# Performance work log

Hardware: AMD Instinct MI355X
Metric: run time of the kernel (lower is better)

The kernel has to match this reference:

```python
import jax, jax.numpy as jnp
import numpy as np

N_NODES = 100000
N_EDGES = 1600000
N_GRAPHS = 1000
X_S = 128
HID = 64


def setup_inputs() -> dict:
    key = jax.random.key(0)
    ks = jax.random.split(key, 12)
    x = jax.random.normal(ks[0], (N_NODES, X_S), dtype=jnp.float32)
    edge_index = jax.random.randint(ks[1], (2, N_EDGES), 0, N_NODES, dtype=jnp.int64)
    batch = jnp.sort(jax.random.randint(ks[2], (N_NODES,), 0, N_GRAPHS, dtype=jnp.int64))
    def lin(k, fin, fout):
        s = 1.0 / np.sqrt(fin)
        kw, kb = jax.random.split(k)
        W = jax.random.uniform(kw, (fin, fout), minval=-s, maxval=s, dtype=jnp.float32)
        b = jax.random.uniform(kb, (fout,), minval=-s, maxval=s, dtype=jnp.float32)
        return W, b
    W1, b1 = lin(ks[3], X_S, HID)
    W2, b2 = lin(ks[4], HID, HID)
    W3, b3 = lin(ks[5], HID, HID)
    Wf, bf = lin(ks[6], HID, 10)
    Wl, bl = lin(ks[7], 10, 1)
    eps1 = jnp.float32(0.37)
    eps2 = jnp.float32(0.72)
    eps3 = jnp.float32(0.11)
    return {"x": x, "edge_index": edge_index, "batch": batch,
            "W1": W1, "b1": b1, "W2": W2, "b2": b2, "W3": W3, "b3": b3,
            "Wf": Wf, "bf": bf, "Wl": Wl, "bl": bl,
            "eps1": eps1, "eps2": eps2, "eps3": eps3}


def _gin_conv(h, src, dst, eps, W, b):
    # GIN: nn((1+eps)*x_i + sum_{j in N(i)} x_j); messages flow src -> dst
    agg = jax.ops.segment_sum(h[src], dst, num_segments=N_NODES)  # [N, d]
    return ((1.0 + eps) * h + agg) @ W + b


def reference(x, edge_index, batch, W1, b1, W2, b2, W3, b3, Wf, bf, Wl, bl,
              eps1, eps2, eps3):
    src, dst = edge_index[0], edge_index[1]
    h = jax.nn.relu(_gin_conv(x, src, dst, eps1, W1, b1))
    h = jax.nn.relu(_gin_conv(h, src, dst, eps2, W2, b2))
    h = jax.nn.relu(_gin_conv(h, src, dst, eps3, W3, b3))
    # global_mean_pool over graph ids
    sums = jax.ops.segment_sum(h, batch, num_segments=N_GRAPHS)        # [G, 64]
    cnts = jax.ops.segment_sum(jnp.ones((N_NODES,), h.dtype), batch,
                               num_segments=N_GRAPHS)                   # [G]
    pooled = sums / jnp.maximum(cnts, 1.0)[:, None]
    out = jax.nn.relu(pooled @ Wf + bf) @ Wl + bl                       # [G, 1]
    return out
```

## Files before the change

### kernel.cpp

```cpp
#include <hip/hip_runtime.h>

#define N_NODES 100000
#define N_EDGES 1600000
#define N_GRAPHS 1000

#define NB_C 782
#define B1   256
#define CHUNK (N_EDGES / B1)
#define MTOT (NB_C * B1)

#define LSTR 68

typedef unsigned int uint32;
typedef unsigned short ushort16;

static __device__ __forceinline__ ushort16 f2bf(float f) {
    uint32 u = __float_as_uint(f);
    u += 0x7fffu + ((u >> 16) & 1u);
    return (ushort16)(u >> 16);
}
static __device__ __forceinline__ uint32 pk2(float a, float b) {
    return (uint32)f2bf(a) | ((uint32)f2bf(b) << 16);
}
static __device__ __forceinline__ void bf2x(uint32 v, float& lo, float& hi) {
    lo = __uint_as_float(v << 16);
    hi = __uint_as_float(v & 0xffff0000u);
}


__global__ __launch_bounds__(256) void count_kernel(
    const int* __restrict__ dst, int* __restrict__ M)
{
    __shared__ int cnt[NB_C];
    int b = blockIdx.x, t = threadIdx.x;
    for (int q = t; q < NB_C; q += 256) cnt[q] = 0;
    __syncthreads();
    int e0 = b * CHUNK;
    for (int e = e0 + t; e < e0 + CHUNK; e += 256)
        atomicAdd(&cnt[dst[e] >> 7], 1);
    __syncthreads();
    for (int q = t; q < NB_C; q += 256) M[q * B1 + b] = cnt[q];
}

#define SCAN_B 1024
#define SCAN_NBLK ((MTOT + SCAN_B - 1) / SCAN_B)

__global__ __launch_bounds__(256) void scanA_kernel(
    const int* __restrict__ in, int* __restrict__ excl, int* __restrict__ bsum)
{
    __shared__ int s[256];
    int b = blockIdx.x, t = threadIdx.x;
    int base = b * SCAN_B + t * 4;
    int v[4];
#pragma unroll
    for (int i = 0; i < 4; ++i) v[i] = (base + i < MTOT) ? in[base + i] : 0;
    int tsum = v[0] + v[1] + v[2] + v[3];
    s[t] = tsum;
    __syncthreads();
    for (int off = 1; off < 256; off <<= 1) {
        int x = (t >= off) ? s[t - off] : 0;
        __syncthreads();
        s[t] += x;
        __syncthreads();
    }
    int run = s[t] - tsum;
#pragma unroll
    for (int i = 0; i < 4; ++i) {
        if (base + i < MTOT) excl[base + i] = run;
        run += v[i];
    }
    if (t == 255) bsum[b] = s[255];
}

__global__ __launch_bounds__(256) void scanB_kernel(int* __restrict__ bsum)
{
    __shared__ int s[256];
    int t = threadIdx.x;
    int v = (t < SCAN_NBLK) ? bsum[t] : 0;
    s[t] = v;
    __syncthreads();
    for (int off = 1; off < 256; off <<= 1) {
        int x = (t >= off) ? s[t - off] : 0;
        __syncthreads();
        s[t] += x;
        __syncthreads();
    }
    if (t < SCAN_NBLK) bsum[t] = s[t] - v;
}

__global__ __launch_bounds__(256) void scanC_kernel(
    const int* __restrict__ excl, const int* __restrict__ bsum,
    int* __restrict__ out)
{
    int b = blockIdx.x, t = threadIdx.x;
    int add = bsum[b];
    int base = b * SCAN_B + t * 4;
#pragma unroll
    for (int i = 0; i < 4; ++i)
        if (base + i < MTOT) out[base + i] = excl[base + i] + add;
}

__global__ __launch_bounds__(256) void scatter_kernel(
    const int* __restrict__ src, const int* __restrict__ dst,
    const int* __restrict__ Ms, uint32* __restrict__ tmp)
{
    __shared__ int cur[NB_C];
    int b = blockIdx.x, t = threadIdx.x;
    for (int q = t; q < NB_C; q += 256) cur[q] = Ms[q * B1 + b];
    __syncthreads();
    int e0 = b * CHUNK;
    for (int e = e0 + t; e < e0 + CHUNK; e += 256) {
        int d = dst[e];
        int q = d >> 7;
        int pos = atomicAdd(&cur[q], 1);
        tmp[pos] = ((uint32)(d & 127) << 17) | (uint32)src[e];
    }
}

__global__ __launch_bounds__(256) void finalize_kernel(
    const uint32* __restrict__ tmp, const int* __restrict__ Ms,
    int* __restrict__ row_off, int* __restrict__ esrc)
{
    __shared__ int cnt[128];
    __shared__ int pref[128];
    __shared__ int cur[128];
    int q = blockIdx.x, t = threadIdx.x;
    int start = Ms[q * B1];
    int end = (q == NB_C - 1) ? N_EDGES : Ms[(q + 1) * B1];

    if (t < 128) cnt[t] = 0;
    __syncthreads();
    for (int e = start + t; e < end; e += 256)
        atomicAdd(&cnt[tmp[e] >> 17], 1);
    __syncthreads();
    if (t < 128) pref[t] = cnt[t];
    __syncthreads();
    for (int off = 1; off < 128; off <<= 1) {
        int x = 0;
        if (t < 128 && t >= off) x = pref[t - off];
        __syncthreads();
        if (t < 128) pref[t] += x;
        __syncthreads();
    }
    if (t < 128) {
        int excl = pref[t] - cnt[t];
        int node = q * 128 + t;
        if (node < N_NODES) row_off[node] = start + excl;
        cur[t] = start + excl;
    }
    if (q == 0 && t == 0) row_off[N_NODES] = N_EDGES;
    __syncthreads();
    for (int e = start + t; e < end; e += 256) {
        uint32 u = tmp[e];
        int pos = atomicAdd(&cur[u >> 17], 1);
        esrc[pos] = (int)(u & 0x1FFFFu);
    }
}

template<int IN>
__global__ __launch_bounds__(256) void gemm_kernel(
    const float* __restrict__ h,
    const float* __restrict__ W,
    ushort16* __restrict__ y)
{
    __shared__ float hs[64 * LSTR];

    const int t = threadIdx.x;
    const int node0 = blockIdx.x * 64;
    const int m = t >> 4;
    const int p = t & 15;

    float4 acc[4];
#pragma unroll
    for (int i = 0; i < 4; ++i) acc[i] = make_float4(0.f, 0.f, 0.f, 0.f);

    for (int kb = 0; kb < IN / 64; ++kb) {
        if (kb) __syncthreads();
        {
            int kc = (t & 15) * 4;
            int rbase = t >> 4;
#pragma unroll
            for (int rr = 0; rr < 4; ++rr) {
                int row = rr * 16 + rbase;
                int node = node0 + row;
                float4 v = make_float4(0.f, 0.f, 0.f, 0.f);
                if (node < N_NODES)
                    v = *(const float4*)&h[(size_t)node * IN + kb * 64 + kc];
                *(float4*)&hs[row * LSTR + kc] = v;
            }
        }
        __syncthreads();

        const float* hb = &hs[(m * 4) * LSTR];
        const float* Wb = W + (size_t)(kb * 64) * 64 + p * 4;
#pragma unroll 4
        for (int kc = 0; kc < 64; kc += 4) {
            float4 hv[4];
#pragma unroll
            for (int i = 0; i < 4; ++i) hv[i] = *(const float4*)&hb[i * LSTR + kc];
            float4 w0 = *(const float4*)&Wb[(kc + 0) * 64];
            float4 w1 = *(const float4*)&Wb[(kc + 1) * 64];
            float4 w2 = *(const float4*)&Wb[(kc + 2) * 64];
            float4 w3 = *(const float4*)&Wb[(kc + 3) * 64];
#pragma unroll
            for (int i = 0; i < 4; ++i) {
                acc[i].x = fmaf(hv[i].x, w0.x, acc[i].x);
                acc[i].y = fmaf(hv[i].x, w0.y, acc[i].y);
                acc[i].z = fmaf(hv[i].x, w0.z, acc[i].z);
                acc[i].w = fmaf(hv[i].x, w0.w, acc[i].w);
                acc[i].x = fmaf(hv[i].y, w1.x, acc[i].x);
                acc[i].y = fmaf(hv[i].y, w1.y, acc[i].y);
                acc[i].z = fmaf(hv[i].y, w1.z, acc[i].z);
                acc[i].w = fmaf(hv[i].y, w1.w, acc[i].w);
                acc[i].x = fmaf(hv[i].z, w2.x, acc[i].x);
                acc[i].y = fmaf(hv[i].z, w2.y, acc[i].y);
                acc[i].z = fmaf(hv[i].z, w2.z, acc[i].z);
                acc[i].w = fmaf(hv[i].z, w2.w, acc[i].w);
                acc[i].x = fmaf(hv[i].w, w3.x, acc[i].x);
                acc[i].y = fmaf(hv[i].w, w3.y, acc[i].y);
                acc[i].z = fmaf(hv[i].w, w3.z, acc[i].z);
                acc[i].w = fmaf(hv[i].w, w3.w, acc[i].w);
            }
        }
    }

#pragma unroll
    for (int i = 0; i < 4; ++i) {
        int node = node0 + m * 4 + i;
        if (node >= N_NODES) continue;
        *(uint2*)&y[(size_t)node * 64 + p * 4] =
            make_uint2(pk2(acc[i].x, acc[i].y), pk2(acc[i].z, acc[i].w));
    }
}

__global__ __launch_bounds__(256) void gemm_bf16_kernel(
    const uint32* __restrict__ hb,
    const float* __restrict__ W,
    ushort16* __restrict__ y)
{
    __shared__ float hs[64 * LSTR];

    const int t = threadIdx.x;
    const int node0 = blockIdx.x * 64;

    {
        int w = t & 7;
        int rbase = t >> 3;
#pragma unroll
        for (int rr = 0; rr < 2; ++rr) {
            int row = rr * 32 + rbase;
            int node = node0 + row;
            uint4 v = make_uint4(0u, 0u, 0u, 0u);
            if (node < N_NODES)
                v = *(const uint4*)&hb[(size_t)node * 32 + w * 4];
            float f[8];
            bf2x(v.x, f[0], f[1]);
            bf2x(v.y, f[2], f[3]);
            bf2x(v.z, f[4], f[5]);
            bf2x(v.w, f[6], f[7]);
            float* o = &hs[row * LSTR + w * 8];
            *(float4*)o       = make_float4(f[0], f[1], f[2], f[3]);
            *(float4*)(o + 4) = make_float4(f[4], f[5], f[6], f[7]);
        }
    }
    __syncthreads();

    const int m = t >> 4;
    const int p = t & 15;
    float4 acc[4];
#pragma unroll
    for (int i = 0; i < 4; ++i) acc[i] = make_float4(0.f, 0.f, 0.f, 0.f);

    const float* hbp = &hs[(m * 4) * LSTR];
    const float* Wb = W + p * 4;
#pragma unroll 4
    for (int kc = 0; kc < 64; kc += 4) {
        float4 hv[4];
#pragma unroll
        for (int i = 0; i < 4; ++i) hv[i] = *(const float4*)&hbp[i * LSTR + kc];
        float4 w0 = *(const float4*)&Wb[(kc + 0) * 64];
        float4 w1 = *(const float4*)&Wb[(kc + 1) * 64];
        float4 w2 = *(const float4*)&Wb[(kc + 2) * 64];
        float4 w3 = *(const float4*)&Wb[(kc + 3) * 64];
#pragma unroll
        for (int i = 0; i < 4; ++i) {
            acc[i].x = fmaf(hv[i].x, w0.x, acc[i].x);
            acc[i].y = fmaf(hv[i].x, w0.y, acc[i].y);
            acc[i].z = fmaf(hv[i].x, w0.z, acc[i].z);
            acc[i].w = fmaf(hv[i].x, w0.w, acc[i].w);
            acc[i].x = fmaf(hv[i].y, w1.x, acc[i].x);
            acc[i].y = fmaf(hv[i].y, w1.y, acc[i].y);
            acc[i].z = fmaf(hv[i].y, w1.z, acc[i].z);
            acc[i].w = fmaf(hv[i].y, w1.w, acc[i].w);
            acc[i].x = fmaf(hv[i].z, w2.x, acc[i].x);
            acc[i].y = fmaf(hv[i].z, w2.y, acc[i].y);
            acc[i].z = fmaf(hv[i].z, w2.z, acc[i].z);
            acc[i].w = fmaf(hv[i].z, w2.w, acc[i].w);
            acc[i].x = fmaf(hv[i].w, w3.x, acc[i].x);
            acc[i].y = fmaf(hv[i].w, w3.y, acc[i].y);
            acc[i].z = fmaf(hv[i].w, w3.z, acc[i].z);
            acc[i].w = fmaf(hv[i].w, w3.w, acc[i].w);
        }
    }

#pragma unroll
    for (int i = 0; i < 4; ++i) {
        int node = node0 + m * 4 + i;
        if (node >= N_NODES) continue;
        *(uint2*)&y[(size_t)node * 64 + p * 4] =
            make_uint2(pk2(acc[i].x, acc[i].y), pk2(acc[i].z, acc[i].w));
    }
}

__global__ __launch_bounds__(256) void aggregate_kernel(
    const uint32* __restrict__ y,
    const int* __restrict__ row_off,
    const int* __restrict__ esrc,
    const float* __restrict__ b,
    const float* __restrict__ eps_p,
    uint32* __restrict__ outb)
{
    int lane = threadIdx.x & 63;
    int wave = threadIdx.x >> 6;
    int g = lane >> 4;
    int j = (lane >> 3) & 1;
    int w = lane & 7;
    int node = blockIdx.x * 16 + wave * 4 + g;

    int s0 = row_off[node], s1 = row_off[node + 1];
    float a[8], c[8];
#pragma unroll
    for (int i = 0; i < 8; ++i) { a[i] = 0.f; c[i] = 0.f; }

    const uint32* yw = y + (size_t)w * 4;
    int e = s0 + j;
    for (; e + 2 < s1; e += 4) {
        int i0 = esrc[e];
        int i1 = esrc[e + 2];
        uint4 v0 = *(const uint4*)&yw[(size_t)i0 * 32];
        uint4 v1 = *(const uint4*)&yw[(size_t)i1 * 32];
        float lo, hi;
        bf2x(v0.x, lo, hi); a[0] += lo; a[1] += hi;
        bf2x(v0.y, lo, hi); a[2] += lo; a[3] += hi;
        bf2x(v0.z, lo, hi); a[4] += lo; a[5] += hi;
        bf2x(v0.w, lo, hi); a[6] += lo; a[7] += hi;
        bf2x(v1.x, lo, hi); c[0] += lo; c[1] += hi;
        bf2x(v1.y, lo, hi); c[2] += lo; c[3] += hi;
        bf2x(v1.z, lo, hi); c[4] += lo; c[5] += hi;
        bf2x(v1.w, lo, hi); c[6] += lo; c[7] += hi;
    }
    if (e < s1) {
        int i0 = esrc[e];
        uint4 v0 = *(const uint4*)&yw[(size_t)i0 * 32];
        float lo, hi;
        bf2x(v0.x, lo, hi); a[0] += lo; a[1] += hi;
        bf2x(v0.y, lo, hi); a[2] += lo; a[3] += hi;
        bf2x(v0.z, lo, hi); a[4] += lo; a[5] += hi;
        bf2x(v0.w, lo, hi); a[6] += lo; a[7] += hi;
    }
#pragma unroll
    for (int i = 0; i < 8; ++i) {
        a[i] += c[i];
        a[i] += __shfl_xor(a[i], 8);
    }

    if (j == 0) {
        uint4 sv = *(const uint4*)&yw[(size_t)node * 32];
        float s[8];
        bf2x(sv.x, s[0], s[1]);
        bf2x(sv.y, s[2], s[3]);
        bf2x(sv.z, s[4], s[5]);
        bf2x(sv.w, s[6], s[7]);
        float ep1 = 1.0f + eps_p[0];
        float4 b0 = *(const float4*)&b[w * 8];
        float4 b1 = *(const float4*)&b[w * 8 + 4];
        float r0 = fmaxf(fmaf(ep1, s[0], a[0]) + b0.x, 0.0f);
        float r1 = fmaxf(fmaf(ep1, s[1], a[1]) + b0.y, 0.0f);
        float r2 = fmaxf(fmaf(ep1, s[2], a[2]) + b0.z, 0.0f);
        float r3 = fmaxf(fmaf(ep1, s[3], a[3]) + b0.w, 0.0f);
        float r4 = fmaxf(fmaf(ep1, s[4], a[4]) + b1.x, 0.0f);
        float r5 = fmaxf(fmaf(ep1, s[5], a[5]) + b1.y, 0.0f);
        float r6 = fmaxf(fmaf(ep1, s[6], a[6]) + b1.z, 0.0f);
        float r7 = fmaxf(fmaf(ep1, s[7], a[7]) + b1.w, 0.0f);
        *(uint4*)&outb[(size_t)node * 32 + w * 4] =
            make_uint4(pk2(r0, r1), pk2(r2, r3), pk2(r4, r5), pk2(r6, r7));
    }
}

__global__ __launch_bounds__(256) void pool_head_kernel(
    const uint32* __restrict__ hb,
    const int* __restrict__ batch,
    const float* __restrict__ Wf,
    const float* __restrict__ bfv,
    const float* __restrict__ Wl,
    const float* __restrict__ blv,
    float* __restrict__ out)
{
    __shared__ float red[4][64];
    __shared__ float pooled[64];
    __shared__ float hid[10];
    int g = blockIdx.x;
    int t = threadIdx.x;
    int lo = 0, hi = N_NODES;
    while (lo < hi) { int mid = (lo + hi) >> 1; if (batch[mid] < g) lo = mid + 1; else hi = mid; }
    int start = lo;
    hi = N_NODES;
    while (lo < hi) { int mid = (lo + hi) >> 1; if (batch[mid] < g + 1) lo = mid + 1; else hi = mid; }
    int end = lo;

    int c = t & 63, nl = t >> 6;
    int wd = c >> 1, odd = c & 1;
    float acc = 0.0f;
    for (int i = start + nl; i < end; i += 4) {
        uint32 u = hb[(size_t)i * 32 + wd];
        acc += __uint_as_float(odd ? (u & 0xffff0000u) : (u << 16));
    }
    red[nl][c] = acc;
    __syncthreads();
    if (t < 64) {
        float cnt = (float)(end - start);
        float inv = 1.0f / fmaxf(cnt, 1.0f);
        pooled[t] = (red[0][t] + red[1][t] + red[2][t] + red[3][t]) * inv;
    }
    __syncthreads();
    if (t < 10) {
        float s = bfv[t];
#pragma unroll
        for (int k = 0; k < 64; ++k) s = fmaf(pooled[k], Wf[k * 10 + t], s);
        hid[t] = fmaxf(s, 0.0f);
    }
    __syncthreads();
    if (t == 0) {
        float s = blv[0];
#pragma unroll
        for (int j = 0; j < 10; ++j) s = fmaf(hid[j], Wl[j], s);
        out[g] = s;
    }
}

extern "C" void kernel_launch(void* const* d_in, const int* in_sizes, int n_in,
                              void* d_out, int out_size, void* d_ws, size_t ws_size,
                              hipStream_t stream)
{
    const float* x     = (const float*)d_in[0];
    const int*   ei    = (const int*)  d_in[1];
    const int*   src   = ei;
    const int*   dst   = ei + N_EDGES;
    const int*   batch = (const int*)  d_in[2];
    const float* W1    = (const float*)d_in[3];
    const float* b1    = (const float*)d_in[4];
    const float* W2    = (const float*)d_in[5];
    const float* b2    = (const float*)d_in[6];
    const float* W3    = (const float*)d_in[7];
    const float* b3    = (const float*)d_in[8];
    const float* Wf    = (const float*)d_in[9];
    const float* bfv   = (const float*)d_in[10];
    const float* Wl    = (const float*)d_in[11];
    const float* blv   = (const float*)d_in[12];
    const float* eps1  = (const float*)d_in[13];
    const float* eps2  = (const float*)d_in[14];
    const float* eps3  = (const float*)d_in[15];

    ushort16* ybA = (ushort16*)d_ws;
    ushort16* ybB = ybA + (size_t)N_NODES * 64;
    int*   ints = (int*)(ybB + (size_t)N_NODES * 64);
    int*   M       = ints;
    int*   Mex     = M + MTOT;
    int*   Ms      = Mex + MTOT;
    int*   bsum    = Ms + MTOT;
    int*   row_off = bsum + 256;
    int*   esrc    = row_off + N_NODES + 1;
    uint32* tmp    = (uint32*)(esrc + N_EDGES);

    count_kernel<<<B1, 256, 0, stream>>>(dst, M);
    scanA_kernel<<<SCAN_NBLK, 256, 0, stream>>>(M, Mex, bsum);
    scanB_kernel<<<1, 256, 0, stream>>>(bsum);
    scanC_kernel<<<SCAN_NBLK, 256, 0, stream>>>(Mex, bsum, Ms);
    scatter_kernel<<<B1, 256, 0, stream>>>(src, dst, Ms, tmp);
    finalize_kernel<<<NB_C, 256, 0, stream>>>(tmp, Ms, row_off, esrc);

    const int gemm_blk = (N_NODES + 63) / 64;
    const int agg_blk  = N_NODES / 16;

    gemm_kernel<128><<<gemm_blk, 256, 0, stream>>>(x, W1, ybA);
    aggregate_kernel<<<agg_blk, 256, 0, stream>>>(
        (const uint32*)ybA, row_off, esrc, b1, eps1, (uint32*)ybB);

    gemm_bf16_kernel<<<gemm_blk, 256, 0, stream>>>((const uint32*)ybB, W2, ybA);
    aggregate_kernel<<<agg_blk, 256, 0, stream>>>(
        (const uint32*)ybA, row_off, esrc, b2, eps2, (uint32*)ybB);

    gemm_bf16_kernel<<<gemm_blk, 256, 0, stream>>>((const uint32*)ybB, W3, ybA);
    aggregate_kernel<<<agg_blk, 256, 0, stream>>>(
        (const uint32*)ybA, row_off, esrc, b3, eps3, (uint32*)ybB);

    pool_head_kernel<<<N_GRAPHS, 256, 0, stream>>>(
        (const uint32*)ybB, batch, Wf, bfv, Wl, blv, (float*)d_out);
}
```

Measured before the change: 352.7 us.

## Use bf16 MFMA instructions for the three GIN layer GEMMs

Replaces the FP32 FMA-based shared-memory GEMM kernels with wave-level 16x16x32 bf16 MFMA kernels that load operands directly into registers. A small preliminary kernel converts and transposes W1..W3 into bf16 workspace buffers so B fragments can be loaded contiguously. The first layer now rounds x to bf16 before multiplying, which adds precision loss, and output stores become scattered 2-byte writes instead of packed vector stores.

```diff
diff --git a/kernel.cpp b/kernel.cpp
--- a/kernel.cpp
+++ b/kernel.cpp
@@ -9,10 +9,10 @@
 #define CHUNK (N_EDGES / B1)
 #define MTOT (NB_C * B1)
 
-#define LSTR 68
-
 typedef unsigned int uint32;
 typedef unsigned short ushort16;
+typedef __attribute__((ext_vector_type(8))) short short8;
+typedef __attribute__((ext_vector_type(4))) float f32x4;
 
 static __device__ __forceinline__ ushort16 f2bf(float f) {
     uint32 u = __float_as_uint(f);
@@ -25,6 +25,33 @@
 static __device__ __forceinline__ void bf2x(uint32 v, float& lo, float& hi) {
     lo = __uint_as_float(v << 16);
     hi = __uint_as_float(v & 0xffff0000u);
+}
+
+union CV8 { uint4 u; short8 s; };
+
+__global__ __launch_bounds__(256) void convw_kernel(
+    const float* __restrict__ W1, const float* __restrict__ W2,
+    const float* __restrict__ W3,
+    ushort16* __restrict__ W1t, ushort16* __restrict__ W2t,
+    ushort16* __restrict__ W3t)
+{
+    int t = threadIdx.x;
+    if (blockIdx.x == 0) {
+        for (int i = t; i < 64 * 128; i += 256) {
+            int j = i >> 7, k = i & 127;
+            W1t[i] = f2bf(W1[k * 64 + j]);
+        }
+    } else if (blockIdx.x == 1) {
+        for (int i = t; i < 64 * 64; i += 256) {
+            int j = i >> 6, k = i & 63;
+            W2t[i] = f2bf(W2[k * 64 + j]);
+        }
+    } else {
+        for (int i = t; i < 64 * 64; i += 256) {
+            int j = i >> 6, k = i & 63;
+            W3t[i] = f2bf(W3[k * 64 + j]);
+        }
+    }
 }
 
 
@@ -157,159 +184,104 @@
     }
 }
 
-template<int IN>
-__global__ __launch_bounds__(256) void gemm_kernel(
-    const float* __restrict__ h,
-    const float* __restrict__ W,
+__global__ __launch_bounds__(256) void gemm1_mfma_kernel(
+    const float* __restrict__ x,
+    const ushort16* __restrict__ Wt,
     ushort16* __restrict__ y)
 {
-    __shared__ float hs[64 * LSTR];
-
-    const int t = threadIdx.x;
-    const int node0 = blockIdx.x * 64;
-    const int m = t >> 4;
-    const int p = t & 15;
-
-    float4 acc[4];
-#pragma unroll
-    for (int i = 0; i < 4; ++i) acc[i] = make_float4(0.f, 0.f, 0.f, 0.f);
-
-    for (int kb = 0; kb < IN / 64; ++kb) {
-        if (kb) __syncthreads();
-        {
-            int kc = (t & 15) * 4;
-            int rbase = t >> 4;
-#pragma unroll
-            for (int rr = 0; rr < 4; ++rr) {
-                int row = rr * 16 + rbase;
-                int node = node0 + row;
-                float4 v = make_float4(0.f, 0.f, 0.f, 0.f);
-                if (node < N_NODES)
-                    v = *(const float4*)&h[(size_t)node * IN + kb * 64 + kc];
-                *(float4*)&hs[row * LSTR + kc] = v;
-            }
-        }
-        __syncthreads();
-
-        const float* hb = &hs[(m * 4) * LSTR];
-        const float* Wb = W + (size_t)(kb * 64) * 64 + p * 4;
-#pragma unroll 4
-        for (int kc = 0; kc < 64; kc += 4) {
-            float4 hv[4];
-#pragma unroll
-            for (int i = 0; i < 4; ++i) hv[i] = *(const float4*)&hb[i * LSTR + kc];
-            float4 w0 = *(const float4*)&Wb[(kc + 0) * 64];
-            float4 w1 = *(const float4*)&Wb[(kc + 1) * 64];
-            float4 w2 = *(const float4*)&Wb[(kc + 2) * 64];
-            float4 w3 = *(const float4*)&Wb[(kc + 3) * 64];
-#pragma unroll
-            for (int i = 0; i < 4; ++i) {
-                acc[i].x = fmaf(hv[i].x, w0.x, acc[i].x);
-                acc[i].y = fmaf(hv[i].x, w0.y, acc[i].y);
-                acc[i].z = fmaf(hv[i].x, w0.z, acc[i].z);
-                acc[i].w = fmaf(hv[i].x, w0.w, acc[i].w);
-                acc[i].x = fmaf(hv[i].y, w1.x, acc[i].x);
-                acc[i].y = fmaf(hv[i].y, w1.y, acc[i].y);
-                acc[i].z = fmaf(hv[i].y, w1.z, acc[i].z);
-                acc[i].w = fmaf(hv[i].y, w1.w, acc[i].w);
-                acc[i].x = fmaf(hv[i].z, w2.x, acc[i].x);
-                acc[i].y = fmaf(hv[i].z, w2.y, acc[i].y);
-                acc[i].z = fmaf(hv[i].z, w2.z, acc[i].z);
-                acc[i].w = fmaf(hv[i].z, w2.w, acc[i].w);
-                acc[i].x = fmaf(hv[i].w, w3.x, acc[i].x);
-                acc[i].y = fmaf(hv[i].w, w3.y, acc[i].y);
-                acc[i].z = fmaf(hv[i].w, w3.z, acc[i].z);
-                acc[i].w = fmaf(hv[i].w, w3.w, acc[i].w);
-            }
-        }
-    }
-
-#pragma unroll
-    for (int i = 0; i < 4; ++i) {
-        int node = node0 + m * 4 + i;
-        if (node >= N_NODES) continue;
-        *(uint2*)&y[(size_t)node * 64 + p * 4] =
-            make_uint2(pk2(acc[i].x, acc[i].y), pk2(acc[i].z, acc[i].w));
-    }
-}
-
-__global__ __launch_bounds__(256) void gemm_bf16_kernel(
-    const uint32* __restrict__ hb,
-    const float* __restrict__ W,
+    int lane = threadIdx.x & 63;
+    int wave = threadIdx.x >> 6;
+    int col = lane & 15, quad = lane >> 4;
+    int node0 = blockIdx.x * 64 + wave * 16;
+    int anode = node0 + col;
+
+    short8 a[4];
+    if (anode < N_NODES) {
+        const float* xr = &x[(size_t)anode * 128 + quad * 8];
+#pragma unroll
+        for (int s = 0; s < 4; ++s) {
+            float4 v0 = *(const float4*)&xr[s * 32];
+            float4 v1 = *(const float4*)&xr[s * 32 + 4];
+            CV8 cv;
+            cv.u = make_uint4(pk2(v0.x, v0.y), pk2(v0.z, v0.w),
+                              pk2(v1.x, v1.y), pk2(v1.z, v1.w));
+            a[s] = cv.s;
+        }
+    } else {
+        short8 z = {0, 0, 0, 0, 0, 0, 0, 0};
+#pragma unroll
+        for (int s = 0; s < 4; ++s) a[s] = z;
+    }
+
+    f32x4 acc[4];
+#pragma unroll
+    for (int nt = 0; nt < 4; ++nt)
+#pragma unroll
+        for (int r = 0; r < 4; ++r) acc[nt][r] = 0.0f;
+
+#pragma unroll
+    for (int nt = 0; nt < 4; ++nt) {
+        const ushort16* wr = &Wt[(size_t)(nt * 16 + col) * 128 + quad * 8];
+#pragma unroll
+        for (int s = 0; s < 4; ++s) {
+            short8 b = *(const short8*)&wr[s * 32];
+            acc[nt] = __builtin_amdgcn_mfma_f32_16x16x32_bf16(a[s], b, acc[nt], 0, 0, 0);
+        }
+    }
+
+#pragma unroll
+    for (int nt = 0; nt < 4; ++nt)
+#pragma unroll
+        for (int r = 0; r < 4; ++r) {
+            int node = node0 + quad * 4 + r;
+            if (node < N_NODES)
+                y[(size_t)node * 64 + nt * 16 + col] = f2bf(acc[nt][r]);
+        }
+}
+
+__global__ __launch_bounds__(256) void gemm_mfma_kernel(
+    const ushort16* __restrict__ hb,
+    const ushort16* __restrict__ Wt,
     ushort16* __restrict__ y)
 {
-    __shared__ float hs[64 * LSTR];
-
-    const int t = threadIdx.x;
-    const int node0 = blockIdx.x * 64;
-
-    {
-        int w = t & 7;
-        int rbase = t >> 3;
-#pragma unroll
-        for (int rr = 0; rr < 2; ++rr) {
-            int row = rr * 32 + rbase;
-            int node = node0 + row;
-            uint4 v = make_uint4(0u, 0u, 0u, 0u);
+    int lane = threadIdx.x & 63;
+    int wave = threadIdx.x >> 6;
+    int col = lane & 15, quad = lane >> 4;
+    int node0 = blockIdx.x * 64 + wave * 16;
+    int anode = node0 + col;
+
+    short8 a0, a1;
+    if (anode < N_NODES) {
+        a0 = *(const short8*)&hb[(size_t)anode * 64 + quad * 8];
+        a1 = *(const short8*)&hb[(size_t)anode * 64 + 32 + quad * 8];
+    } else {
+        short8 z = {0, 0, 0, 0, 0, 0, 0, 0};
+        a0 = z; a1 = z;
+    }
+
+    f32x4 acc[4];
+#pragma unroll
+    for (int nt = 0; nt < 4; ++nt)
+#pragma unroll
+        for (int r = 0; r < 4; ++r) acc[nt][r] = 0.0f;
+
+#pragma unroll
+    for (int nt = 0; nt < 4; ++nt) {
+        const ushort16* wr = &Wt[(size_t)(nt * 16 + col) * 64 + quad * 8];
+        short8 b0 = *(const short8*)&wr[0];
+        short8 b1 = *(const short8*)&wr[32];
+        acc[nt] = __builtin_amdgcn_mfma_f32_16x16x32_bf16(a0, b0, acc[nt], 0, 0, 0);
+        acc[nt] = __builtin_amdgcn_mfma_f32_16x16x32_bf16(a1, b1, acc[nt], 0, 0, 0);
+    }
+
+#pragma unroll
+    for (int nt = 0; nt < 4; ++nt)
+#pragma unroll
+        for (int r = 0; r < 4; ++r) {
+            int node = node0 + quad * 4 + r;
             if (node < N_NODES)
-                v = *(const uint4*)&hb[(size_t)node * 32 + w * 4];
-            float f[8];
-            bf2x(v.x, f[0], f[1]);
-            bf2x(v.y, f[2], f[3]);
-            bf2x(v.z, f[4], f[5]);
-            bf2x(v.w, f[6], f[7]);
-            float* o = &hs[row * LSTR + w * 8];
-            *(float4*)o       = make_float4(f[0], f[1], f[2], f[3]);
-            *(float4*)(o + 4) = make_float4(f[4], f[5], f[6], f[7]);
-        }
-    }
-    __syncthreads();
-
-    const int m = t >> 4;
-    const int p = t & 15;
-    float4 acc[4];
-#pragma unroll
-    for (int i = 0; i < 4; ++i) acc[i] = make_float4(0.f, 0.f, 0.f, 0.f);
-
-    const float* hbp = &hs[(m * 4) * LSTR];
-    const float* Wb = W + p * 4;
-#pragma unroll 4
-    for (int kc = 0; kc < 64; kc += 4) {
-        float4 hv[4];
-#pragma unroll
-        for (int i = 0; i < 4; ++i) hv[i] = *(const float4*)&hbp[i * LSTR + kc];
-        float4 w0 = *(const float4*)&Wb[(kc + 0) * 64];
-        float4 w1 = *(const float4*)&Wb[(kc + 1) * 64];
-        float4 w2 = *(const float4*)&Wb[(kc + 2) * 64];
-        float4 w3 = *(const float4*)&Wb[(kc + 3) * 64];
-#pragma unroll
-        for (int i = 0; i < 4; ++i) {
-            acc[i].x = fmaf(hv[i].x, w0.x, acc[i].x);
-            acc[i].y = fmaf(hv[i].x, w0.y, acc[i].y);
-            acc[i].z = fmaf(hv[i].x, w0.z, acc[i].z);
-            acc[i].w = fmaf(hv[i].x, w0.w, acc[i].w);
-            acc[i].x = fmaf(hv[i].y, w1.x, acc[i].x);
-            acc[i].y = fmaf(hv[i].y, w1.y, acc[i].y);
-            acc[i].z = fmaf(hv[i].y, w1.z, acc[i].z);
-            acc[i].w = fmaf(hv[i].y, w1.w, acc[i].w);
-            acc[i].x = fmaf(hv[i].z, w2.x, acc[i].x);
-            acc[i].y = fmaf(hv[i].z, w2.y, acc[i].y);
-            acc[i].z = fmaf(hv[i].z, w2.z, acc[i].z);
-            acc[i].w = fmaf(hv[i].z, w2.w, acc[i].w);
-            acc[i].x = fmaf(hv[i].w, w3.x, acc[i].x);
-            acc[i].y = fmaf(hv[i].w, w3.y, acc[i].y);
-            acc[i].z = fmaf(hv[i].w, w3.z, acc[i].z);
-            acc[i].w = fmaf(hv[i].w, w3.w, acc[i].w);
-        }
-    }
-
-#pragma unroll
-    for (int i = 0; i < 4; ++i) {
-        int node = node0 + m * 4 + i;
-        if (node >= N_NODES) continue;
-        *(uint2*)&y[(size_t)node * 64 + p * 4] =
-            make_uint2(pk2(acc[i].x, acc[i].y), pk2(acc[i].z, acc[i].w));
-    }
+                y[(size_t)node * 64 + nt * 16 + col] = f2bf(acc[nt][r]);
+        }
 }
 
 __global__ __launch_bounds__(256) void aggregate_kernel(
@@ -471,6 +443,14 @@
     int*   row_off = bsum + 256;
     int*   esrc    = row_off + N_NODES + 1;
     uint32* tmp    = (uint32*)(esrc + N_EDGES);
+    ushort16* W1t = (ushort16*)(((uintptr_t)(tmp + N_EDGES) + 255) & ~(uintptr_t)255);
+    ushort16* W2t = W1t + 64 * 128;
+    ushort16* W3t = W2t + 64 * 64;
+
+    const int gemm_blk = (N_NODES + 63) / 64;
+    const int agg_blk  = N_NODES / 16;
+
+    convw_kernel<<<3, 256, 0, stream>>>(W1, W2, W3, W1t, W2t, W3t);
 
     count_kernel<<<B1, 256, 0, stream>>>(dst, M);
     scanA_kernel<<<SCAN_NBLK, 256, 0, stream>>>(M, Mex, bsum);
@@ -479,18 +459,15 @@
     scatter_kernel<<<B1, 256, 0, stream>>>(src, dst, Ms, tmp);
     finalize_kernel<<<NB_C, 256, 0, stream>>>(tmp, Ms, row_off, esrc);
 
-    const int gemm_blk = (N_NODES + 63) / 64;
-    const int agg_blk  = N_NODES / 16;
-
-    gemm_kernel<128><<<gemm_blk, 256, 0, stream>>>(x, W1, ybA);
+    gemm1_mfma_kernel<<<gemm_blk, 256, 0, stream>>>(x, W1t, ybA);
     aggregate_kernel<<<agg_blk, 256, 0, stream>>>(
         (const uint32*)ybA, row_off, esrc, b1, eps1, (uint32*)ybB);
 
-    gemm_bf16_kernel<<<gemm_blk, 256, 0, stream>>>((const uint32*)ybB, W2, ybA);
+    gemm_mfma_kernel<<<gemm_blk, 256, 0, stream>>>(ybB, W2t, ybA);
     aggregate_kernel<<<agg_blk, 256, 0, stream>>>(
         (const uint32*)ybA, row_off, esrc, b2, eps2, (uint32*)ybB);
 
-    gemm_bf16_kernel<<<gemm_blk, 256, 0, stream>>>((const uint32*)ybB, W3, ybA);
+    gemm_mfma_kernel<<<gemm_blk, 256, 0, stream>>>(ybB, W3t, ybA);
     aggregate_kernel<<<agg_blk, 256, 0, stream>>>(
         (const uint32*)ybA, row_off, esrc, b3, eps3, (uint32*)ybB);
 
```

After: 330.4 us. 6.3% less time.
